# Performance work log

Measured on AMD Instinct MI355X. Metric: run time of the kernel, lower is better.

## Reference

```python
import jax, jax.numpy as jnp
import numpy as np

GAMMA = 0.01
INFER_STEP = 4
C, B, G, S, L = 8, 32, 2048, 32, 3


def softor(x, axis, gamma=GAMMA):
    # gamma-weighted soft-or: gamma * logsumexp(x/gamma); renormalize if max > 1
    lse = gamma * jax.nn.logsumexp(x / gamma, axis=axis)
    m = jnp.max(lse)
    return jnp.where(m > 1.0, lse / m, lse)


def clause_fn(I_i, x):
    # I_i: [G, S, L] int indices into atom axis; x: [B, G]
    gathered = jnp.take(x, I_i, axis=1)        # [B, G, S, L]
    body = jnp.prod(gathered, axis=3)          # [B, G, S] (AND over body literals)
    return softor(body, axis=2)                # [B, G]   (OR over substitutions)


def setup_inputs() -> dict:
    key = jax.random.key(0)
    k1, k2 = jax.random.split(key)
    x = jax.random.uniform(k1, (B, G), dtype=jnp.float32)
    I = jax.random.randint(k2, (C, G, S, L), 0, G)
    return {"x": x, "I": I}


def reference(x, I):
    # R: [C, B, G] per-clause valuations, initialized from x
    R = jnp.broadcast_to(x[None], (C, B, G))
    r = jax.vmap(clause_fn)  # map over clause axis of I and R
    for _ in range(INFER_STEP):
        R = softor(jnp.stack([R, r(I, R)], axis=1), axis=1)
    return R
```

## Files before the change

kernel.cpp:

```cpp
#include <hip/hip_runtime.h>
#include <hip/hip_bf16.h>

#define C_ 8
#define B_ 32
#define G_ 2048
#define S_ 32
#define L_ 3
#define GB_ (G_ * B_)


#define OFF_BUF0 0
#define OFF_BUF1 524288
#define OFF_MAX  1048576
#define OFF_GMAX (OFF_MAX + 512)
#define OFF_XT   (OFF_MAX + 640)
#define ZERO_FLOATS 576

#define K_SCALE 144.26950408889634f
#define GLN2 0.0069314718055994531f

#define EXP2F(x) __builtin_amdgcn_exp2f(x)
#define LOG2F(x) __builtin_amdgcn_logf(x)

__device__ __forceinline__ void atomicMaxPos(float* a, float v) {
    atomicMax((unsigned*)a, __float_as_uint(v));
}

__global__ __launch_bounds__(1024) void k_init(const float* __restrict__ x,
                                               float* __restrict__ xT,
                                               float* __restrict__ maxs) {
    __shared__ float sT[32 * 33];
    const int tid = threadIdx.x, bid = blockIdx.x;
    const int g0 = bid * 32;
    sT[(tid & 31) * 33 + (tid >> 5)] = x[(tid >> 5) * G_ + g0 + (tid & 31)];
    __syncthreads();
    {
        const int gloc = tid >> 5, b = tid & 31;
        xT[(b >> 2) * (G_ * 4) + (g0 + gloc) * 4 + (b & 3)] = sT[gloc * 33 + b];
    }
    if (bid == 0 && tid < ZERO_FLOATS) maxs[tid] = 0.0f;
}

__global__ __launch_bounds__(256, 2) void k_clause(const float* __restrict__ Rbase,
                                                   int cstride,
                                                   const int* __restrict__ I,
                                                   float* __restrict__ r_out,
                                                   const float* __restrict__ gmax_prev,
                                                   float* __restrict__ cmax_step) {
    __shared__ float sR[G_ * 4];
    __shared__ float sRed[4];

    const int tid = threadIdx.x;
    const int bid = blockIdx.x;
    const int c = bid >> 6;
    const int bh = (bid >> 3) & 7;
    const int gs = bid & 7;

    const float gm = gmax_prev ? gmax_prev[0] : 0.0f;
    const float sc = (gm > 1.0f) ? (1.0f / gm) : 1.0f;

    {
        const float4* src = (const float4*)(Rbase + c * cstride + bh * (G_ * 4));
        float4* dst = (float4*)sR;
#pragma unroll
        for (int k = 0; k < 8; ++k) {
            float4 v = src[tid + k * 256];
            v.x *= sc; v.y *= sc; v.z *= sc; v.w *= sc;
            dst[tid + k * 256] = v;
        }
    }
    __syncthreads();

    const int bh2 = tid & 1;
    const float2* sR2 = (const float2*)sR + bh2;

    float blockm = -1e30f;

#pragma unroll 1
    for (int pass = 0; pass < 2; ++pass) {
        const int row = gs * 256 + pass * 128 + (tid >> 1);
        const int4* p = (const int4*)(I + (c * G_ + row) * 96);

        float2 lm[8], pp[8];
#pragma unroll
        for (int ch = 0; ch < 8; ++ch) {
            const int4 qa = p[ch * 3 + 0], qb = p[ch * 3 + 1], qc = p[ch * 3 + 2];
            const float2 v0 = sR2[qa.x << 1], v1 = sR2[qa.y << 1], v2 = sR2[qa.z << 1];
            const float2 v3 = sR2[qa.w << 1], v4 = sR2[qb.x << 1], v5 = sR2[qb.y << 1];
            const float2 v6 = sR2[qb.z << 1], v7 = sR2[qb.w << 1], v8 = sR2[qc.x << 1];
            const float2 v9 = sR2[qc.y << 1], va = sR2[qc.z << 1], vb = sR2[qc.w << 1];
            float2 b0, b1, b2, b3;
            b0.x = v0.x * v1.x * (v2.x * K_SCALE);  b0.y = v0.y * v1.y * (v2.y * K_SCALE);
            b1.x = v3.x * v4.x * (v5.x * K_SCALE);  b1.y = v3.y * v4.y * (v5.y * K_SCALE);
            b2.x = v6.x * v7.x * (v8.x * K_SCALE);  b2.y = v6.y * v7.y * (v8.y * K_SCALE);
            b3.x = v9.x * va.x * (vb.x * K_SCALE);  b3.y = v9.y * va.y * (vb.y * K_SCALE);
            lm[ch].x = fmaxf(fmaxf(b0.x, b1.x), fmaxf(b2.x, b3.x));
            lm[ch].y = fmaxf(fmaxf(b0.y, b1.y), fmaxf(b2.y, b3.y));
            pp[ch].x = EXP2F(b0.x - lm[ch].x) + EXP2F(b1.x - lm[ch].x) +
                       EXP2F(b2.x - lm[ch].x) + EXP2F(b3.x - lm[ch].x);
            pp[ch].y = EXP2F(b0.y - lm[ch].y) + EXP2F(b1.y - lm[ch].y) +
                       EXP2F(b2.y - lm[ch].y) + EXP2F(b3.y - lm[ch].y);
        }
        float2 M;
        M.x = fmaxf(fmaxf(fmaxf(lm[0].x, lm[1].x), fmaxf(lm[2].x, lm[3].x)),
                    fmaxf(fmaxf(lm[4].x, lm[5].x), fmaxf(lm[6].x, lm[7].x)));
        M.y = fmaxf(fmaxf(fmaxf(lm[0].y, lm[1].y), fmaxf(lm[2].y, lm[3].y)),
                    fmaxf(fmaxf(lm[4].y, lm[5].y), fmaxf(lm[6].y, lm[7].y)));
        float2 sum = make_float2(0.0f, 0.0f);
#pragma unroll
        for (int ch = 0; ch < 8; ++ch) {
            sum.x += pp[ch].x * EXP2F(lm[ch].x - M.x);
            sum.y += pp[ch].y * EXP2F(lm[ch].y - M.y);
        }
        float2 lse;
        lse.x = GLN2 * (M.x + LOG2F(sum.x));
        lse.y = GLN2 * (M.y + LOG2F(sum.y));

        *(float2*)(r_out + ((c * 8 + bh) * G_ + row) * 4 + bh2 * 2) = lse;
        blockm = fmaxf(blockm, fmaxf(lse.x, lse.y));
    }

    float m = blockm;
#pragma unroll
    for (int o = 32; o; o >>= 1) m = fmaxf(m, __shfl_xor(m, o, 64));
    const int lane = tid & 63, wv = tid >> 6;
    if (lane == 0) sRed[wv] = m;
    __syncthreads();
    if (tid == 0) {
        float a = fmaxf(fmaxf(sRed[0], sRed[1]), fmaxf(sRed[2], sRed[3]));
        atomicMaxPos(&cmax_step[c * 16], a);
    }
}

__global__ __launch_bounds__(256, 8) void k_combine(const float* __restrict__ Rold,
                                                    int mask,
                                                    const float* __restrict__ r_in,
                                                    float* __restrict__ Rnew,
                                                    const float* __restrict__ gmax_prev,
                                                    const float* __restrict__ cmax_step,
                                                    float* __restrict__ gmax_out) {
    __shared__ float sRed[4];
    const int tid = threadIdx.x;
    const int i4 = (blockIdx.x * 256 + tid) * 4;
    const int c = i4 >> 16;

    const float gm = gmax_prev ? gmax_prev[0] : 0.0f;
    const float sc = (gm > 1.0f) ? (1.0f / gm) : 1.0f;
    const float cmv = cmax_step[c * 16];
    const float scr = (cmv > 1.0f) ? (1.0f / cmv) : 1.0f;

    const float4 Ro = *(const float4*)(Rold + (i4 & mask));
    const float4 rv = *(const float4*)(r_in + i4);
    float4 o;
    {
        float Rn = Ro.x * sc, rn = rv.x * scr;
        float M = fmaxf(Rn, rn), mn = fminf(Rn, rn);
        o.x = M + 0.01f * __logf(1.0f + __expf((mn - M) * 100.0f));
    }
    {
        float Rn = Ro.y * sc, rn = rv.y * scr;
        float M = fmaxf(Rn, rn), mn = fminf(Rn, rn);
        o.y = M + 0.01f * __logf(1.0f + __expf((mn - M) * 100.0f));
    }
    {
        float Rn = Ro.z * sc, rn = rv.z * scr;
        float M = fmaxf(Rn, rn), mn = fminf(Rn, rn);
        o.z = M + 0.01f * __logf(1.0f + __expf((mn - M) * 100.0f));
    }
    {
        float Rn = Ro.w * sc, rn = rv.w * scr;
        float M = fmaxf(Rn, rn), mn = fminf(Rn, rn);
        o.w = M + 0.01f * __logf(1.0f + __expf((mn - M) * 100.0f));
    }
    *(float4*)(Rnew + i4) = o;

    float mm = fmaxf(fmaxf(o.x, o.y), fmaxf(o.z, o.w));
#pragma unroll
    for (int off = 32; off; off >>= 1) mm = fmaxf(mm, __shfl_xor(mm, off, 64));
    const int lane = tid & 63, wv = tid >> 6;
    if (lane == 0) sRed[wv] = mm;
    __syncthreads();
    if (tid == 0) {
        float a = fmaxf(fmaxf(sRed[0], sRed[1]), fmaxf(sRed[2], sRed[3]));
        atomicMaxPos(gmax_out, a);
    }
}

__global__ __launch_bounds__(256) void k_out(const float* __restrict__ buf0,
                                             const float* __restrict__ gmaxslot,
                                             float* __restrict__ out) {
    __shared__ float sT[32 * 65];
    const int bid = blockIdx.x;
    const int c = bid >> 5;
    const int g0 = (bid & 31) << 6;
    const int tid = threadIdx.x;

    const float gm = gmaxslot[0];
    const float sc = (gm > 1.0f) ? (1.0f / gm) : 1.0f;

    const int r = tid >> 2, w = tid & 3;
#pragma unroll
    for (int k = 0; k < 8; ++k) {
        sT[(k * 4 + w) * 65 + r] = buf0[((c * 8 + k) * G_ + g0 + r) * 4 + w] * sc;
    }
    __syncthreads();
#pragma unroll
    for (int k = 0; k < 8; ++k) {
        const int j = tid + k * 256;
        const int b = j >> 6, gg = j & 63;
        out[(c * B_ + b) * G_ + g0 + gg] = sT[b * 65 + gg];
    }
}

extern "C" void kernel_launch(void* const* d_in, const int* in_sizes, int n_in,
                              void* d_out, int out_size, void* d_ws, size_t ws_size,
                              hipStream_t stream) {
    const float* x = (const float*)d_in[0];
    const int* I = (const int*)d_in[1];
    float* out = (float*)d_out;
    float* ws = (float*)d_ws;

    float* buf0 = ws + OFF_BUF0;
    float* buf1 = ws + OFF_BUF1;
    float* maxs = ws + OFF_MAX;
    float* gmax = ws + OFF_GMAX;
    float* xT = ws + OFF_XT;

    k_init<<<64, 1024, 0, stream>>>(x, xT, maxs);

    for (int t = 0; t < 4; ++t) {
        const float* Rsrc = (t == 0) ? xT : buf0;
        const int cs = (t == 0) ? 0 : GB_;
        const float* gprev = (t == 0) ? nullptr : (gmax + (t - 1) * 16);
        float* cstep = maxs + t * 128;
        const int mask = (t == 0) ? (GB_ - 1) : 0x7FFFFFFF;

        k_clause<<<512, 256, 0, stream>>>(Rsrc, cs, I, buf1, gprev, cstep);
        k_combine<<<512, 256, 0, stream>>>(Rsrc, mask, buf1, buf0, gprev, cstep,
                                           gmax + t * 16);
    }

    k_out<<<256, 256, 0, stream>>>(buf0, gmax + 48, out);
}
```

Before: 95.72 us.

## Fold x transpose into first clause/combine and use float4 per-thread rows

Removes the separate k_init transpose kernel. The first iteration's clause and combine kernels now read x directly in its original layout (xmode), and the max buffer is zeroed with hipMemsetAsync. The clause kernel also changes from 2 threads per row over 2 passes to one thread per row handling all 4 batch lanes with float4 LDS gathers. This halves the gather instruction count and loads each index once per row. In exchange, register pressure per thread roughly doubles, and the first step's loads are strided and uncoalesced.

```diff
diff --git a/kernel.cpp b/kernel.cpp
--- a/kernel.cpp
+++ b/kernel.cpp
@@ -13,7 +13,6 @@
 #define OFF_BUF1 524288
 #define OFF_MAX  1048576
 #define OFF_GMAX (OFF_MAX + 512)
-#define OFF_XT   (OFF_MAX + 640)
 #define ZERO_FLOATS 576
 
 #define K_SCALE 144.26950408889634f
@@ -26,23 +25,29 @@
     atomicMax((unsigned*)a, __float_as_uint(v));
 }
 
-__global__ __launch_bounds__(1024) void k_init(const float* __restrict__ x,
-                                               float* __restrict__ xT,
-                                               float* __restrict__ maxs) {
-    __shared__ float sT[32 * 33];
-    const int tid = threadIdx.x, bid = blockIdx.x;
-    const int g0 = bid * 32;
-    sT[(tid & 31) * 33 + (tid >> 5)] = x[(tid >> 5) * G_ + g0 + (tid & 31)];
-    __syncthreads();
-    {
-        const int gloc = tid >> 5, b = tid & 31;
-        xT[(b >> 2) * (G_ * 4) + (g0 + gloc) * 4 + (b & 3)] = sT[gloc * 33 + b];
-    }
-    if (bid == 0 && tid < ZERO_FLOATS) maxs[tid] = 0.0f;
+__device__ __forceinline__ float4 body3(float4 a, float4 b, float4 c) {
+    float4 r;
+    r.x = a.x * b.x * (c.x * K_SCALE);
+    r.y = a.y * b.y * (c.y * K_SCALE);
+    r.z = a.z * b.z * (c.z * K_SCALE);
+    r.w = a.w * b.w * (c.w * K_SCALE);
+    return r;
+}
+__device__ __forceinline__ float4 fmax4v(float4 a, float4 b) {
+    float4 r;
+    r.x = fmaxf(a.x, b.x); r.y = fmaxf(a.y, b.y);
+    r.z = fmaxf(a.z, b.z); r.w = fmaxf(a.w, b.w);
+    return r;
+}
+__device__ __forceinline__ float4 exp2m(float4 a, float4 m) {
+    float4 r;
+    r.x = EXP2F(a.x - m.x); r.y = EXP2F(a.y - m.y);
+    r.z = EXP2F(a.z - m.z); r.w = EXP2F(a.w - m.w);
+    return r;
 }
 
 __global__ __launch_bounds__(256, 2) void k_clause(const float* __restrict__ Rbase,
-                                                   int cstride,
+                                                   int xmode,
                                                    const int* __restrict__ I,
                                                    float* __restrict__ r_out,
                                                    const float* __restrict__ gmax_prev,
@@ -59,8 +64,17 @@
     const float gm = gmax_prev ? gmax_prev[0] : 0.0f;
     const float sc = (gm > 1.0f) ? (1.0f / gm) : 1.0f;
 
-    {
-        const float4* src = (const float4*)(Rbase + c * cstride + bh * (G_ * 4));
+    if (xmode) {
+        const int j = tid >> 6;
+        const int g0 = tid & 63;
+        const float* xr = Rbase + (bh * 4 + j) * G_;
+#pragma unroll
+        for (int k = 0; k < 32; ++k) {
+            const int g = g0 + 64 * k;
+            sR[g * 4 + j] = xr[g];
+        }
+    } else {
+        const float4* src = (const float4*)(Rbase + c * GB_ + bh * (G_ * 4));
         float4* dst = (float4*)sR;
 #pragma unroll
         for (int k = 0; k < 8; ++k) {
@@ -71,56 +85,46 @@
     }
     __syncthreads();
 
-    const int bh2 = tid & 1;
-    const float2* sR2 = (const float2*)sR + bh2;
-
-    float blockm = -1e30f;
-
-#pragma unroll 1
-    for (int pass = 0; pass < 2; ++pass) {
-        const int row = gs * 256 + pass * 128 + (tid >> 1);
-        const int4* p = (const int4*)(I + (c * G_ + row) * 96);
-
-        float2 lm[8], pp[8];
-#pragma unroll
-        for (int ch = 0; ch < 8; ++ch) {
-            const int4 qa = p[ch * 3 + 0], qb = p[ch * 3 + 1], qc = p[ch * 3 + 2];
-            const float2 v0 = sR2[qa.x << 1], v1 = sR2[qa.y << 1], v2 = sR2[qa.z << 1];
-            const float2 v3 = sR2[qa.w << 1], v4 = sR2[qb.x << 1], v5 = sR2[qb.y << 1];
-            const float2 v6 = sR2[qb.z << 1], v7 = sR2[qb.w << 1], v8 = sR2[qc.x << 1];
-            const float2 v9 = sR2[qc.y << 1], va = sR2[qc.z << 1], vb = sR2[qc.w << 1];
-            float2 b0, b1, b2, b3;
-            b0.x = v0.x * v1.x * (v2.x * K_SCALE);  b0.y = v0.y * v1.y * (v2.y * K_SCALE);
-            b1.x = v3.x * v4.x * (v5.x * K_SCALE);  b1.y = v3.y * v4.y * (v5.y * K_SCALE);
-            b2.x = v6.x * v7.x * (v8.x * K_SCALE);  b2.y = v6.y * v7.y * (v8.y * K_SCALE);
-            b3.x = v9.x * va.x * (vb.x * K_SCALE);  b3.y = v9.y * va.y * (vb.y * K_SCALE);
-            lm[ch].x = fmaxf(fmaxf(b0.x, b1.x), fmaxf(b2.x, b3.x));
-            lm[ch].y = fmaxf(fmaxf(b0.y, b1.y), fmaxf(b2.y, b3.y));
-            pp[ch].x = EXP2F(b0.x - lm[ch].x) + EXP2F(b1.x - lm[ch].x) +
-                       EXP2F(b2.x - lm[ch].x) + EXP2F(b3.x - lm[ch].x);
-            pp[ch].y = EXP2F(b0.y - lm[ch].y) + EXP2F(b1.y - lm[ch].y) +
-                       EXP2F(b2.y - lm[ch].y) + EXP2F(b3.y - lm[ch].y);
-        }
-        float2 M;
-        M.x = fmaxf(fmaxf(fmaxf(lm[0].x, lm[1].x), fmaxf(lm[2].x, lm[3].x)),
-                    fmaxf(fmaxf(lm[4].x, lm[5].x), fmaxf(lm[6].x, lm[7].x)));
-        M.y = fmaxf(fmaxf(fmaxf(lm[0].y, lm[1].y), fmaxf(lm[2].y, lm[3].y)),
-                    fmaxf(fmaxf(lm[4].y, lm[5].y), fmaxf(lm[6].y, lm[7].y)));
-        float2 sum = make_float2(0.0f, 0.0f);
-#pragma unroll
-        for (int ch = 0; ch < 8; ++ch) {
-            sum.x += pp[ch].x * EXP2F(lm[ch].x - M.x);
-            sum.y += pp[ch].y * EXP2F(lm[ch].y - M.y);
-        }
-        float2 lse;
-        lse.x = GLN2 * (M.x + LOG2F(sum.x));
-        lse.y = GLN2 * (M.y + LOG2F(sum.y));
-
-        *(float2*)(r_out + ((c * 8 + bh) * G_ + row) * 4 + bh2 * 2) = lse;
-        blockm = fmaxf(blockm, fmaxf(lse.x, lse.y));
-    }
-
-    float m = blockm;
+    const float4* sR4 = (const float4*)sR;
+    const int row = gs * 256 + tid;
+    const int4* p = (const int4*)(I + (c * G_ + row) * 96);
+
+    float4 lm[8], pp[8];
+#pragma unroll
+    for (int ch = 0; ch < 8; ++ch) {
+        const int4 qa = p[ch * 3 + 0], qb = p[ch * 3 + 1], qc = p[ch * 3 + 2];
+        const float4 b0 = body3(sR4[qa.x], sR4[qa.y], sR4[qa.z]);
+        const float4 b1 = body3(sR4[qa.w], sR4[qb.x], sR4[qb.y]);
+        const float4 b2 = body3(sR4[qb.z], sR4[qb.w], sR4[qc.x]);
+        const float4 b3 = body3(sR4[qc.y], sR4[qc.z], sR4[qc.w]);
+        const float4 l = fmax4v(fmax4v(b0, b1), fmax4v(b2, b3));
+        const float4 e0 = exp2m(b0, l), e1 = exp2m(b1, l);
+        const float4 e2 = exp2m(b2, l), e3 = exp2m(b3, l);
+        float4 s;
+        s.x = e0.x + e1.x + e2.x + e3.x;
+        s.y = e0.y + e1.y + e2.y + e3.y;
+        s.z = e0.z + e1.z + e2.z + e3.z;
+        s.w = e0.w + e1.w + e2.w + e3.w;
+        lm[ch] = l; pp[ch] = s;
+    }
+    float4 M = fmax4v(fmax4v(fmax4v(lm[0], lm[1]), fmax4v(lm[2], lm[3])),
+                      fmax4v(fmax4v(lm[4], lm[5]), fmax4v(lm[6], lm[7])));
+    float4 sum = make_float4(0.f, 0.f, 0.f, 0.f);
+#pragma unroll
+    for (int ch = 0; ch < 8; ++ch) {
+        const float4 w = exp2m(lm[ch], M);
+        sum.x += pp[ch].x * w.x; sum.y += pp[ch].y * w.y;
+        sum.z += pp[ch].z * w.z; sum.w += pp[ch].w * w.w;
+    }
+    float4 lse;
+    lse.x = GLN2 * (M.x + LOG2F(sum.x));
+    lse.y = GLN2 * (M.y + LOG2F(sum.y));
+    lse.z = GLN2 * (M.z + LOG2F(sum.z));
+    lse.w = GLN2 * (M.w + LOG2F(sum.w));
+
+    *(float4*)(r_out + ((c * 8 + bh) * G_ + row) * 4) = lse;
+
+    float m = fmaxf(fmaxf(lse.x, lse.y), fmaxf(lse.z, lse.w));
 #pragma unroll
     for (int o = 32; o; o >>= 1) m = fmaxf(m, __shfl_xor(m, o, 64));
     const int lane = tid & 63, wv = tid >> 6;
@@ -133,7 +137,7 @@
 }
 
 __global__ __launch_bounds__(256, 8) void k_combine(const float* __restrict__ Rold,
-                                                    int mask,
+                                                    int xmode,
                                                     const float* __restrict__ r_in,
                                                     float* __restrict__ Rnew,
                                                     const float* __restrict__ gmax_prev,
@@ -149,7 +153,18 @@
     const float cmv = cmax_step[c * 16];
     const float scr = (cmv > 1.0f) ? (1.0f / cmv) : 1.0f;
 
-    const float4 Ro = *(const float4*)(Rold + (i4 & mask));
+    float4 Ro;
+    if (xmode) {
+        const int w = i4 & (GB_ - 1);
+        const int bq = w >> 13;
+        const int g = (w & 8191) >> 2;
+        Ro.x = Rold[(bq * 4 + 0) * G_ + g];
+        Ro.y = Rold[(bq * 4 + 1) * G_ + g];
+        Ro.z = Rold[(bq * 4 + 2) * G_ + g];
+        Ro.w = Rold[(bq * 4 + 3) * G_ + g];
+    } else {
+        Ro = *(const float4*)(Rold + i4);
+    }
     const float4 rv = *(const float4*)(r_in + i4);
     float4 o;
     {
@@ -224,19 +239,17 @@
     float* buf1 = ws + OFF_BUF1;
     float* maxs = ws + OFF_MAX;
     float* gmax = ws + OFF_GMAX;
-    float* xT = ws + OFF_XT;
-
-    k_init<<<64, 1024, 0, stream>>>(x, xT, maxs);
+
+    hipMemsetAsync(ws + OFF_MAX, 0, ZERO_FLOATS * sizeof(float), stream);
 
     for (int t = 0; t < 4; ++t) {
-        const float* Rsrc = (t == 0) ? xT : buf0;
-        const int cs = (t == 0) ? 0 : GB_;
+        const float* Rsrc = (t == 0) ? x : buf0;
+        const int xmode = (t == 0) ? 1 : 0;
         const float* gprev = (t == 0) ? nullptr : (gmax + (t - 1) * 16);
         float* cstep = maxs + t * 128;
-        const int mask = (t == 0) ? (GB_ - 1) : 0x7FFFFFFF;
-
-        k_clause<<<512, 256, 0, stream>>>(Rsrc, cs, I, buf1, gprev, cstep);
-        k_combine<<<512, 256, 0, stream>>>(Rsrc, mask, buf1, buf0, gprev, cstep,
+
+        k_clause<<<512, 256, 0, stream>>>(Rsrc, xmode, I, buf1, gprev, cstep);
+        k_combine<<<512, 256, 0, stream>>>(Rsrc, xmode, buf1, buf0, gprev, cstep,
                                            gmax + t * 16);
     }
 
```

Result: no change. 94.44 us (-1.3%).
